# Optimization experiments

Hardware: AMD Instinct MI355X
Metric: run time of the kernel (lower is better)

## Reference

```python
import jax, jax.numpy as jnp
import numpy as np

B, S, C, H, D = 4, 2048, 512, 8, 64
EPS = 1e-5
SCALE = D ** -0.5


def layer_norm(x, w, b):
    m = jnp.mean(x, axis=-1, keepdims=True)
    v = jnp.var(x, axis=-1, keepdims=True)
    return (x - m) * jax.lax.rsqrt(v + EPS) * w + b


def setup_inputs() -> dict:
    key = jax.random.key(0)
    ks = jax.random.split(key, 7)
    s = 0.02
    return {
        "x": jax.random.normal(ks[0], (B, S, C), jnp.float32),
        "Wq": jax.random.normal(ks[1], (C, H * D), jnp.float32) * s,
        "Wk": jax.random.normal(ks[2], (C, H * D), jnp.float32) * s,
        "Wv": jax.random.normal(ks[3], (C, H * D), jnp.float32) * s,
        "Wo": jax.random.normal(ks[4], (H * D, C), jnp.float32) * s,
        "ln1_w": jnp.ones((C,), jnp.float32), "ln1_b": jnp.zeros((C,), jnp.float32),
        "ff_ln1_w": jnp.ones((C,), jnp.float32), "ff_ln1_b": jnp.zeros((C,), jnp.float32),
        "ff_w1": jax.random.normal(ks[5], (C, C), jnp.float32) * s, "ff_b1": jnp.zeros((C,), jnp.float32),
        "ff_ln2_w": jnp.ones((C,), jnp.float32), "ff_ln2_b": jnp.zeros((C,), jnp.float32),
        "ff_w2": jax.random.normal(ks[6], (C, C), jnp.float32) * s, "ff_b2": jnp.zeros((C,), jnp.float32),
        "ln2_w": jnp.ones((C,), jnp.float32), "ln2_b": jnp.zeros((C,), jnp.float32),
    }


def causal_attention(x, Wq, Wk, Wv, Wo):
    # Mathematically identical to the bucketed memory-efficient attention:
    # online-softmax bucketing changes compute order, not the result.
    q = (x @ Wq).reshape(B, S, H, D).transpose(0, 2, 1, 3)  # [B,H,S,D]
    k = (x @ Wk).reshape(B, S, H, D).transpose(0, 2, 1, 3)
    v = (x @ Wv).reshape(B, S, H, D).transpose(0, 2, 1, 3)
    scores = jnp.einsum('bhqd,bhkd->bhqk', q, k) * SCALE  # [B,H,S,S]
    causal = jnp.tril(jnp.ones((S, S), bool))
    scores = jnp.where(causal, scores, jnp.finfo(scores.dtype).min)
    attn = jax.nn.softmax(scores, axis=-1)
    out = jnp.einsum('bhqk,bhkd->bhqd', attn, v)
    out = out.transpose(0, 2, 1, 3).reshape(B, S, H * D)
    return out @ Wo


def reference(x, Wq, Wk, Wv, Wo, ln1_w, ln1_b, ff_ln1_w, ff_ln1_b, ff_w1, ff_b1,
              ff_ln2_w, ff_ln2_b, ff_w2, ff_b2, ln2_w, ln2_b):
    a = causal_attention(x, Wq, Wk, Wv, Wo)
    x_ln = layer_norm(a + x, ln1_w, ln1_b)
    h = layer_norm(x_ln, ff_ln1_w, ff_ln1_b) @ ff_w1 + ff_b1
    h = layer_norm(h, ff_ln2_w, ff_ln2_b) @ ff_w2 + ff_b2
    return layer_norm(h + x_ln, ln2_w, ln2_b)
```

## Files before the change

### kernel.cpp

```cpp
#include <hip/hip_runtime.h>

#define B_ 4
#define S_ 2048
#define C_ 512
#define H_ 8
#define D_ 64
#define M_ 8192

typedef short s8v __attribute__((ext_vector_type(8)));
typedef short s4v __attribute__((ext_vector_type(4)));
typedef float f4v __attribute__((ext_vector_type(4)));
typedef unsigned short u16;
typedef unsigned int u32;

__device__ __forceinline__ u16 f2b(float f) {
    u32 u = __builtin_bit_cast(u32, f);
    u = u + 0x7fffu + ((u >> 16) & 1u);
    return (u16)(u >> 16);
}

__device__ __forceinline__ void gl2lds16(const void* g, void* l) {
    __builtin_amdgcn_global_load_lds(
        (const __attribute__((address_space(1))) void*)g,
        (__attribute__((address_space(3))) void*)l, 16, 0, 0);
}

__global__ __launch_bounds__(256) void conv_k(const float* __restrict__ s,
                                              u16* __restrict__ d) {
    const int i = (blockIdx.x * 256 + threadIdx.x) * 4;
    const float4 v = *(const float4*)&s[i];
    ushort4 o;
    o.x = f2b(v.x); o.y = f2b(v.y); o.z = f2b(v.z); o.w = f2b(v.w);
    *(ushort4*)&d[i] = o;
}

__global__ __launch_bounds__(256) void trconv6_k(const float* __restrict__ s0,
                                                 const float* __restrict__ s1,
                                                 const float* __restrict__ s2,
                                                 const float* __restrict__ s3,
                                                 const float* __restrict__ s4,
                                                 const float* __restrict__ s5,
                                                 u16* __restrict__ d0,
                                                 u16* __restrict__ d1,
                                                 u16* __restrict__ d2,
                                                 u16* __restrict__ d3,
                                                 u16* __restrict__ d4,
                                                 u16* __restrict__ d5)
{
    const float* W; u16* Wt;
    switch (blockIdx.z) {
        case 0: W = s0; Wt = d0; break;
        case 1: W = s1; Wt = d1; break;
        case 2: W = s2; Wt = d2; break;
        case 3: W = s3; Wt = d3; break;
        case 4: W = s4; Wt = d4; break;
        default: W = s5; Wt = d5; break;
    }
    __shared__ float t[32][33];
    const int tx = threadIdx.x & 31, ty = threadIdx.x >> 5;
    const int n0 = blockIdx.x * 32, k0 = blockIdx.y * 32;
    #pragma unroll
    for (int i = 0; i < 4; ++i)
        t[ty + i * 8][tx] = W[(size_t)(k0 + ty + i * 8) * C_ + n0 + tx];
    __syncthreads();
    #pragma unroll
    for (int i = 0; i < 4; ++i)
        Wt[(size_t)(n0 + ty + i * 8) * C_ + k0 + tx] = f2b(t[tx][ty + i * 8]);
}

__global__ __launch_bounds__(256) void vtr_k(const u16* __restrict__ V,
                                             u16* __restrict__ Vt) {
    __shared__ u16 T[64][72];
    const int tid = threadIdx.x;
    const int s0 = blockIdx.x * 64, h = blockIdx.y, b = blockIdx.z;
    const u16* src = V + ((size_t)b * S_) * C_ + h * D_;
    #pragma unroll
    for (int it = 0; it < 2; ++it) {
        const int r = (tid >> 3) + it * 32;
        const int c = (tid & 7) * 8;
        *(s8v*)&T[r][c] = *(const s8v*)&src[(size_t)(s0 + r) * C_ + c];
    }
    __syncthreads();
    u16* dst = Vt + ((size_t)(b * H_ + h)) * D_ * S_;
    #pragma unroll
    for (int it = 0; it < 2; ++it) {
        const int d = (tid >> 3) + it * 32;
        const int sl = (tid & 7) * 8;
        s4v lo, hi;
        #pragma unroll
        for (int i = 0; i < 4; ++i) lo[i] = (short)T[sl + i][d];
        #pragma unroll
        for (int i = 0; i < 4; ++i) hi[i] = (short)T[sl + 4 + i][d];
        const int span = s0 + (sl & ~31);
        const int g0 = (sl & 31) >> 2;
        const int xw = d & 7;
        u16* drow = dst + (size_t)d * S_ + span;
        *(s4v*)&drow[((g0 ^ xw) << 2)]       = lo;
        *(s4v*)&drow[(((g0 + 1) ^ xw) << 2)] = hi;
    }
}

template <bool OB>
__global__ __launch_bounds__(256) void gemm_k(const u16* __restrict__ A,
                                              const u16* __restrict__ Bt,
                                              const float* __restrict__ bias,
                                              void* __restrict__ outv)
{
    __shared__ u16 As[2][8][16][32];
    __shared__ u16 Bs[2][8][16][32];
    const int tid = threadIdx.x;
    const int lane = tid & 63, w = tid >> 6;
    const int q4 = lane >> 4, l16 = lane & 15;
    const int wr = w >> 1, wc = w & 1;
    const int bm = blockIdx.y * 128, bn = blockIdx.x * 128;
    const int lr = lane >> 2, lc = (lane & 3) * 8;

    f4v acc[4][4];
    #pragma unroll
    for (int i = 0; i < 4; ++i)
        #pragma unroll
        for (int j = 0; j < 4; ++j) acc[i][j] = (f4v){0.f, 0.f, 0.f, 0.f};

    #pragma unroll
    for (int r = 0; r < 2; ++r) {
        const int seg = r * 4 + w;
        const int row = seg * 16 + lr;
        gl2lds16(A  + (size_t)(bm + row) * C_ + lc, (char*)As + seg * 1024);
        gl2lds16(Bt + (size_t)(bn + row) * C_ + lc, (char*)Bs + seg * 1024);
    }

    for (int kt = 0; kt < 16; ++kt) {
        __syncthreads();
        const int buf = kt & 1;
        if (kt < 15) {
            const int nb = buf ^ 1, k0 = (kt + 1) * 32;
            #pragma unroll
            for (int r = 0; r < 2; ++r) {
                const int seg = r * 4 + w;
                const int row = seg * 16 + lr;
                gl2lds16(A  + (size_t)(bm + row) * C_ + k0 + lc, (char*)As + nb * 8192 + seg * 1024);
                gl2lds16(Bt + (size_t)(bn + row) * C_ + k0 + lc, (char*)Bs + nb * 8192 + seg * 1024);
            }
        }
        s8v a[4], bf[4];
        #pragma unroll
        for (int i = 0; i < 4; ++i) {
            const int row = wr * 64 + i * 16 + l16;
            a[i] = *(const s8v*)&As[buf][row >> 4][row & 15][q4 * 8];
        }
        #pragma unroll
        for (int j = 0; j < 4; ++j) {
            const int row = wc * 64 + j * 16 + l16;
            bf[j] = *(const s8v*)&Bs[buf][row >> 4][row & 15][q4 * 8];
        }
        #pragma unroll
        for (int i = 0; i < 4; ++i)
            #pragma unroll
            for (int j = 0; j < 4; ++j)
                acc[i][j] = __builtin_amdgcn_mfma_f32_16x16x32_bf16(a[i], bf[j], acc[i][j], 0, 0, 0);
    }

    #pragma unroll
    for (int j = 0; j < 4; ++j) {
        const int n = bn + wc * 64 + j * 16 + l16;
        const float bj = bias ? bias[n] : 0.0f;
        #pragma unroll
        for (int i = 0; i < 4; ++i) {
            const int m = bm + wr * 64 + i * 16 + q4 * 4;
            #pragma unroll
            for (int reg = 0; reg < 4; ++reg) {
                const float vv = acc[i][j][reg] + bj;
                if constexpr (OB) ((u16*)outv)[(size_t)(m + reg) * C_ + n] = f2b(vv);
                else              ((float*)outv)[(size_t)(m + reg) * C_ + n] = vv;
            }
        }
    }
}

__global__ __launch_bounds__(256) void qkv_k(const u16* __restrict__ A,
                                             const u16* __restrict__ Wq,
                                             const u16* __restrict__ Wk,
                                             const u16* __restrict__ Wv,
                                             u16* __restrict__ oq,
                                             u16* __restrict__ ok,
                                             u16* __restrict__ ov)
{
    __shared__ u16 As[2][8][16][32];
    __shared__ u16 Bs[2][8][16][32];
    const int tid = threadIdx.x;
    const int lane = tid & 63, w = tid >> 6;
    const int q4 = lane >> 4, l16 = lane & 15;
    const int wr = w >> 1, wc = w & 1;
    const int nt = blockIdx.x, which = nt >> 2;
    const u16* Bt = which == 0 ? Wq : (which == 1 ? Wk : Wv);
    u16* outp = which == 0 ? oq : (which == 1 ? ok : ov);
    const int bm = blockIdx.y * 128, bn = (nt & 3) * 128;
    const int lr = lane >> 2, lc = (lane & 3) * 8;

    f4v acc[4][4];
    #pragma unroll
    for (int i = 0; i < 4; ++i)
        #pragma unroll
        for (int j = 0; j < 4; ++j) acc[i][j] = (f4v){0.f, 0.f, 0.f, 0.f};

    #pragma unroll
    for (int r = 0; r < 2; ++r) {
        const int seg = r * 4 + w;
        const int row = seg * 16 + lr;
        gl2lds16(A  + (size_t)(bm + row) * C_ + lc, (char*)As + seg * 1024);
        gl2lds16(Bt + (size_t)(bn + row) * C_ + lc, (char*)Bs + seg * 1024);
    }
    for (int kt = 0; kt < 16; ++kt) {
        __syncthreads();
        const int buf = kt & 1;
        if (kt < 15) {
            const int nb = buf ^ 1, k0 = (kt + 1) * 32;
            #pragma unroll
            for (int r = 0; r < 2; ++r) {
                const int seg = r * 4 + w;
                const int row = seg * 16 + lr;
                gl2lds16(A  + (size_t)(bm + row) * C_ + k0 + lc, (char*)As + nb * 8192 + seg * 1024);
                gl2lds16(Bt + (size_t)(bn + row) * C_ + k0 + lc, (char*)Bs + nb * 8192 + seg * 1024);
            }
        }
        s8v a[4], bf[4];
        #pragma unroll
        for (int i = 0; i < 4; ++i) {
            const int row = wr * 64 + i * 16 + l16;
            a[i] = *(const s8v*)&As[buf][row >> 4][row & 15][q4 * 8];
        }
        #pragma unroll
        for (int j = 0; j < 4; ++j) {
            const int row = wc * 64 + j * 16 + l16;
            bf[j] = *(const s8v*)&Bs[buf][row >> 4][row & 15][q4 * 8];
        }
        #pragma unroll
        for (int i = 0; i < 4; ++i)
            #pragma unroll
            for (int j = 0; j < 4; ++j)
                acc[i][j] = __builtin_amdgcn_mfma_f32_16x16x32_bf16(a[i], bf[j], acc[i][j], 0, 0, 0);
    }
    #pragma unroll
    for (int j = 0; j < 4; ++j) {
        const int n = bn + wc * 64 + j * 16 + l16;
        #pragma unroll
        for (int i = 0; i < 4; ++i) {
            const int m = bm + wr * 64 + i * 16 + q4 * 4;
            #pragma unroll
            for (int reg = 0; reg < 4; ++reg)
                outp[(size_t)(m + reg) * C_ + n] = f2b(acc[i][j][reg]);
        }
    }
}

template <bool OB>
__global__ __launch_bounds__(256) void ln_k(const float* __restrict__ in,
                                            const float* __restrict__ res,
                                            const float* __restrict__ w,
                                            const float* __restrict__ bb,
                                            void* __restrict__ outv)
{
    const int lane = threadIdx.x & 63;
    const int row  = blockIdx.x * 4 + (threadIdx.x >> 6);
    const float* p = in + (size_t)row * C_;
    float4 v0 = *(const float4*)&p[lane * 4];
    float4 v1 = *(const float4*)&p[256 + lane * 4];
    if (res) {
        const float* rp = res + (size_t)row * C_;
        const float4 r0 = *(const float4*)&rp[lane * 4];
        const float4 r1 = *(const float4*)&rp[256 + lane * 4];
        v0.x += r0.x; v0.y += r0.y; v0.z += r0.z; v0.w += r0.w;
        v1.x += r1.x; v1.y += r1.y; v1.z += r1.z; v1.w += r1.w;
    }
    float s  = v0.x + v0.y + v0.z + v0.w + v1.x + v1.y + v1.z + v1.w;
    float ss = v0.x*v0.x + v0.y*v0.y + v0.z*v0.z + v0.w*v0.w
             + v1.x*v1.x + v1.y*v1.y + v1.z*v1.z + v1.w*v1.w;
    #pragma unroll
    for (int off = 32; off >= 1; off >>= 1) {
        s  += __shfl_xor(s, off);
        ss += __shfl_xor(ss, off);
    }
    const float mean = s * (1.0f / C_);
    const float var  = ss * (1.0f / C_) - mean * mean;
    const float rstd = rsqrtf(var + 1e-5f);

    const float4 w0 = *(const float4*)&w[lane * 4];
    const float4 w1 = *(const float4*)&w[256 + lane * 4];
    const float4 b0 = *(const float4*)&bb[lane * 4];
    const float4 b1 = *(const float4*)&bb[256 + lane * 4];
    float4 o0, o1;
    o0.x = (v0.x - mean) * rstd * w0.x + b0.x;
    o0.y = (v0.y - mean) * rstd * w0.y + b0.y;
    o0.z = (v0.z - mean) * rstd * w0.z + b0.z;
    o0.w = (v0.w - mean) * rstd * w0.w + b0.w;
    o1.x = (v1.x - mean) * rstd * w1.x + b1.x;
    o1.y = (v1.y - mean) * rstd * w1.y + b1.y;
    o1.z = (v1.z - mean) * rstd * w1.z + b1.z;
    o1.w = (v1.w - mean) * rstd * w1.w + b1.w;
    if constexpr (OB) {
        u16* op = (u16*)outv + (size_t)row * C_;
        ushort4 u0, u1;
        u0.x = f2b(o0.x); u0.y = f2b(o0.y); u0.z = f2b(o0.z); u0.w = f2b(o0.w);
        u1.x = f2b(o1.x); u1.y = f2b(o1.y); u1.z = f2b(o1.z); u1.w = f2b(o1.w);
        *(ushort4*)&op[lane * 4]       = u0;
        *(ushort4*)&op[256 + lane * 4] = u1;
    } else {
        float* op = (float*)outv + (size_t)row * C_;
        *(float4*)&op[lane * 4]       = o0;
        *(float4*)&op[256 + lane * 4] = o1;
    }
}

__global__ __launch_bounds__(256) void attn_k(const u16* __restrict__ Q,
                                              const u16* __restrict__ K,
                                              const u16* __restrict__ Vt,
                                              u16* __restrict__ O)
{
    __shared__ u16 Ks[2][2][64][32];
    __shared__ u16 Vs[2][2][64][32];
    const int tid = threadIdx.x;
    const int lane = tid & 63, w = tid >> 6;
    const int q4 = lane >> 4, l16 = lane & 15;
    const int x = blockIdx.x, h = blockIdx.y, b = blockIdx.z;
    const int qb = (x & 1) ? 31 - (x >> 1) : (x >> 1);
    const size_t base  = ((size_t)b * S_) * C_ + h * D_;
    const size_t basev = ((size_t)(b * H_ + h)) * D_ * S_;
    const int lr = lane >> 2, lc = (lane & 3) * 8;

    s8v qf[2];
    #pragma unroll
    for (int kh = 0; kh < 2; ++kh)
        qf[kh] = *(const s8v*)&Q[base + (size_t)(qb * 64 + w * 16 + l16) * C_ + kh * 32 + q4 * 8];

    #pragma unroll
    for (int r = 0; r < 2; ++r) {
        const int seg = r * 4 + w;
        const int row = (seg & 3) * 16 + lr;
        const int kh = seg >> 2;
        gl2lds16(K  + base  + (size_t)row * C_ + kh * 32 + lc, (char*)Ks + seg * 1024);
        gl2lds16(Vt + basev + (size_t)row * S_ + kh * 32 + lc, (char*)Vs + seg * 1024);
    }

    f4v o[4];
    float lp[4] = {0.f, 0.f, 0.f, 0.f};
    #pragma unroll
    for (int j = 0; j < 4; ++j) o[j] = (f4v){0.f, 0.f, 0.f, 0.f};

    const int qrow = w * 16 + l16;
    for (int kb = 0; kb <= qb; ++kb) {
        __syncthreads();
        const int buf = kb & 1;
        if (kb < qb) {
            const int nb = buf ^ 1, kn = kb + 1;
            #pragma unroll
            for (int r = 0; r < 2; ++r) {
                const int seg = r * 4 + w;
                const int row = (seg & 3) * 16 + lr;
                const int kh = seg >> 2;
                gl2lds16(K  + base  + (size_t)(kn * 64 + row) * C_ + kh * 32 + lc,
                         (char*)Ks + nb * 8192 + seg * 1024);
                gl2lds16(Vt + basev + (size_t)row * S_ + kn * 64 + kh * 32 + lc,
                         (char*)Vs + nb * 8192 + seg * 1024);
            }
        }

        f4v sc[4];
        #pragma unroll
        for (int j = 0; j < 4; ++j) sc[j] = (f4v){0.f, 0.f, 0.f, 0.f};
        #pragma unroll
        for (int kh = 0; kh < 2; ++kh) {
            #pragma unroll
            for (int j = 0; j < 4; ++j) {
                const s8v kf = *(const s8v*)&Ks[buf][kh][j * 16 + l16][q4 * 8];
                sc[j] = __builtin_amdgcn_mfma_f32_16x16x32_bf16(kf, qf[kh], sc[j], 0, 0, 0);
            }
        }

        const bool diag = (kb == qb);
        s4v pa[4];
        #pragma unroll
        for (int j = 0; j < 4; ++j) {
            float ps = 0.0f;
            #pragma unroll
            for (int reg = 0; reg < 4; ++reg) {
                float t = fmaf(sc[j][reg], 0.18033688011112043f, -11.541560327111707f);
                if (diag && (j * 16 + q4 * 4 + reg) > qrow) t = -128.0f;
                const float p = exp2f(t);
                ps += p;
                pa[j][reg] = (short)(__builtin_bit_cast(u32, p) >> 16);
            }
            lp[j] += ps;
        }

        #pragma unroll
        for (int c = 0; c < 4; ++c) {
            const int gh = (((c & 1) * 4 + q4) ^ (l16 & 7)) * 4;
            #pragma unroll
            for (int dj = 0; dj < 4; ++dj) {
                const s4v vb = *(const s4v*)&Vs[buf][c >> 1][dj * 16 + l16][gh];
                o[dj] = __builtin_amdgcn_mfma_f32_16x16x16bf16_1k(pa[c], vb, o[dj], 0, 0, 0);
            }
        }
    }

    float lt = (lp[0] + lp[1]) + (lp[2] + lp[3]);
    lt += __shfl_xor(lt, 16);
    lt += __shfl_xor(lt, 32);
    #pragma unroll
    for (int reg = 0; reg < 4; ++reg) {
        const float inv = 1.0f / __shfl(lt, q4 * 4 + reg);
        const size_t rowoff = base + (size_t)(qb * 64 + w * 16 + q4 * 4 + reg) * C_;
        #pragma unroll
        for (int dj = 0; dj < 4; ++dj)
            O[rowoff + dj * 16 + l16] = f2b(o[dj][reg] * inv);
    }
}

extern "C" void kernel_launch(void* const* d_in, const int* in_sizes, int n_in,
                              void* d_out, int out_size, void* d_ws, size_t ws_size,
                              hipStream_t stream)
{
    const float* x       = (const float*)d_in[0];
    const float* Wq      = (const float*)d_in[1];
    const float* Wk      = (const float*)d_in[2];
    const float* Wv      = (const float*)d_in[3];
    const float* Wo      = (const float*)d_in[4];
    const float* ln1_w   = (const float*)d_in[5];
    const float* ln1_b   = (const float*)d_in[6];
    const float* ffln1_w = (const float*)d_in[7];
    const float* ffln1_b = (const float*)d_in[8];
    const float* ff_w1   = (const float*)d_in[9];
    const float* ff_b1   = (const float*)d_in[10];
    const float* ffln2_w = (const float*)d_in[11];
    const float* ffln2_b = (const float*)d_in[12];
    const float* ff_w2   = (const float*)d_in[13];
    const float* ff_b2   = (const float*)d_in[14];
    const float* ln2_w   = (const float*)d_in[15];
    const float* ln2_b   = (const float*)d_in[16];
    float* out = (float*)d_out;

    const size_t MC = (size_t)M_ * C_;
    const size_t WW = (size_t)C_ * C_;
    u16* xb   = (u16*)d_ws;
    u16* WqT  = xb + MC;
    u16* WkT  = WqT + WW;
    u16* WvT  = WkT + WW;
    u16* WoT  = WvT + WW;
    u16* W1T  = WoT + WW;
    u16* W2T  = W1T + WW;
    u16* qbuf = W2T + WW;
    u16* kbuf = qbuf + MC;
    u16* vbuf = kbuf + MC;
    u16* vtbuf= vbuf + MC;
    u16* abuf = xb;
    float* tf  = (float*)qbuf;
    float* xln = (float*)vbuf;
    u16*   lnb = xb;

    const dim3 gg(C_ / 128, M_ / 128);
    const dim3 gq(12, M_ / 128);
    const dim3 ga(32, H_, B_);
    const dim3 gv(S_ / 64, H_, B_);
    const dim3 gt(16, 16, 6);
    const int  gl = M_ / 4;

    conv_k<<<MC / 1024, 256, 0, stream>>>(x, xb);
    trconv6_k<<<gt, 256, 0, stream>>>(Wq, Wk, Wv, Wo, ff_w1, ff_w2,
                                      WqT, WkT, WvT, WoT, W1T, W2T);

    qkv_k<<<gq, 256, 0, stream>>>(xb, WqT, WkT, WvT, qbuf, kbuf, vbuf);
    vtr_k<<<gv, 256, 0, stream>>>(vbuf, vtbuf);
    attn_k<<<ga, 256, 0, stream>>>(qbuf, kbuf, vtbuf, abuf);
    gemm_k<false><<<gg, 256, 0, stream>>>(abuf, WoT, nullptr, tf);
    ln_k<false><<<gl, 256, 0, stream>>>(tf, x, ln1_w, ln1_b, xln);
    ln_k<true><<<gl, 256, 0, stream>>>(xln, nullptr, ffln1_w, ffln1_b, lnb);
    gemm_k<false><<<gg, 256, 0, stream>>>(lnb, W1T, ff_b1, tf);
    ln_k<true><<<gl, 256, 0, stream>>>(tf, nullptr, ffln2_w, ffln2_b, lnb);
    gemm_k<false><<<gg, 256, 0, stream>>>(lnb, W2T, ff_b2, tf);
    ln_k<false><<<gl, 256, 0, stream>>>(tf, xln, ln2_w, ln2_b, out);
}
```

Measured before the change: 270.5 us.

## Fuse V transpose into QKV, merge LayerNorms, retile GEMM and attention

The QKV kernel now writes V directly in the swizzled transposed layout, which removes the separate vtr_k kernel. Two consecutive LayerNorms are fused into one kernel that writes both the fp32 residual and the bf16 normalized output. The output GEMMs use 64x128 tiles, doubling the grid for better CU occupancy. Attention now handles 128 query rows per block as two 16-row groups per wave so each K/V tile is reused twice, and only the diagonal tiles apply the causal mask. The trade-offs are more registers per attention wave, fewer attention blocks, and scattered 8-byte writes for V.

```diff
diff --git a/kernel.cpp b/kernel.cpp
--- a/kernel.cpp
+++ b/kernel.cpp
@@ -68,65 +68,31 @@
         Wt[(size_t)(n0 + ty + i * 8) * C_ + k0 + tx] = f2b(t[tx][ty + i * 8]);
 }
 
-__global__ __launch_bounds__(256) void vtr_k(const u16* __restrict__ V,
-                                             u16* __restrict__ Vt) {
-    __shared__ u16 T[64][72];
-    const int tid = threadIdx.x;
-    const int s0 = blockIdx.x * 64, h = blockIdx.y, b = blockIdx.z;
-    const u16* src = V + ((size_t)b * S_) * C_ + h * D_;
-    #pragma unroll
-    for (int it = 0; it < 2; ++it) {
-        const int r = (tid >> 3) + it * 32;
-        const int c = (tid & 7) * 8;
-        *(s8v*)&T[r][c] = *(const s8v*)&src[(size_t)(s0 + r) * C_ + c];
-    }
-    __syncthreads();
-    u16* dst = Vt + ((size_t)(b * H_ + h)) * D_ * S_;
-    #pragma unroll
-    for (int it = 0; it < 2; ++it) {
-        const int d = (tid >> 3) + it * 32;
-        const int sl = (tid & 7) * 8;
-        s4v lo, hi;
-        #pragma unroll
-        for (int i = 0; i < 4; ++i) lo[i] = (short)T[sl + i][d];
-        #pragma unroll
-        for (int i = 0; i < 4; ++i) hi[i] = (short)T[sl + 4 + i][d];
-        const int span = s0 + (sl & ~31);
-        const int g0 = (sl & 31) >> 2;
-        const int xw = d & 7;
-        u16* drow = dst + (size_t)d * S_ + span;
-        *(s4v*)&drow[((g0 ^ xw) << 2)]       = lo;
-        *(s4v*)&drow[(((g0 + 1) ^ xw) << 2)] = hi;
-    }
-}
-
 template <bool OB>
 __global__ __launch_bounds__(256) void gemm_k(const u16* __restrict__ A,
                                               const u16* __restrict__ Bt,
                                               const float* __restrict__ bias,
                                               void* __restrict__ outv)
 {
-    __shared__ u16 As[2][8][16][32];
+    __shared__ u16 As[2][4][16][32];
     __shared__ u16 Bs[2][8][16][32];
     const int tid = threadIdx.x;
     const int lane = tid & 63, w = tid >> 6;
     const int q4 = lane >> 4, l16 = lane & 15;
-    const int wr = w >> 1, wc = w & 1;
-    const int bm = blockIdx.y * 128, bn = blockIdx.x * 128;
+    const int bm = blockIdx.y * 64, bn = blockIdx.x * 128;
     const int lr = lane >> 2, lc = (lane & 3) * 8;
 
-    f4v acc[4][4];
+    f4v acc[4][2];
     #pragma unroll
     for (int i = 0; i < 4; ++i)
         #pragma unroll
-        for (int j = 0; j < 4; ++j) acc[i][j] = (f4v){0.f, 0.f, 0.f, 0.f};
-
+        for (int j = 0; j < 2; ++j) acc[i][j] = (f4v){0.f, 0.f, 0.f, 0.f};
+
+    gl2lds16(A + (size_t)(bm + w * 16 + lr) * C_ + lc, (char*)As + w * 1024);
     #pragma unroll
     for (int r = 0; r < 2; ++r) {
-        const int seg = r * 4 + w;
-        const int row = seg * 16 + lr;
-        gl2lds16(A  + (size_t)(bm + row) * C_ + lc, (char*)As + seg * 1024);
-        gl2lds16(Bt + (size_t)(bn + row) * C_ + lc, (char*)Bs + seg * 1024);
+        const int seg = w * 2 + r;
+        gl2lds16(Bt + (size_t)(bn + seg * 16 + lr) * C_ + lc, (char*)Bs + seg * 1024);
     }
 
     for (int kt = 0; kt < 16; ++kt) {
@@ -134,39 +100,37 @@
         const int buf = kt & 1;
         if (kt < 15) {
             const int nb = buf ^ 1, k0 = (kt + 1) * 32;
+            gl2lds16(A + (size_t)(bm + w * 16 + lr) * C_ + k0 + lc,
+                     (char*)As + nb * 4096 + w * 1024);
             #pragma unroll
             for (int r = 0; r < 2; ++r) {
-                const int seg = r * 4 + w;
-                const int row = seg * 16 + lr;
-                gl2lds16(A  + (size_t)(bm + row) * C_ + k0 + lc, (char*)As + nb * 8192 + seg * 1024);
-                gl2lds16(Bt + (size_t)(bn + row) * C_ + k0 + lc, (char*)Bs + nb * 8192 + seg * 1024);
-            }
-        }
-        s8v a[4], bf[4];
+                const int seg = w * 2 + r;
+                gl2lds16(Bt + (size_t)(bn + seg * 16 + lr) * C_ + k0 + lc,
+                         (char*)Bs + nb * 8192 + seg * 1024);
+            }
+        }
+        s8v a[4], bfr[2];
+        #pragma unroll
+        for (int i = 0; i < 4; ++i) a[i] = *(const s8v*)&As[buf][i][l16][q4 * 8];
+        #pragma unroll
+        for (int j = 0; j < 2; ++j) {
+            const int row = w * 32 + j * 16 + l16;
+            bfr[j] = *(const s8v*)&Bs[buf][row >> 4][row & 15][q4 * 8];
+        }
+        #pragma unroll
+        for (int i = 0; i < 4; ++i)
+            #pragma unroll
+            for (int j = 0; j < 2; ++j)
+                acc[i][j] = __builtin_amdgcn_mfma_f32_16x16x32_bf16(a[i], bfr[j], acc[i][j], 0, 0, 0);
+    }
+
+    #pragma unroll
+    for (int j = 0; j < 2; ++j) {
+        const int n = bn + w * 32 + j * 16 + l16;
+        const float bj = bias ? bias[n] : 0.0f;
         #pragma unroll
         for (int i = 0; i < 4; ++i) {
-            const int row = wr * 64 + i * 16 + l16;
-            a[i] = *(const s8v*)&As[buf][row >> 4][row & 15][q4 * 8];
-        }
-        #pragma unroll
-        for (int j = 0; j < 4; ++j) {
-            const int row = wc * 64 + j * 16 + l16;
-            bf[j] = *(const s8v*)&Bs[buf][row >> 4][row & 15][q4 * 8];
-        }
-        #pragma unroll
-        for (int i = 0; i < 4; ++i)
-            #pragma unroll
-            for (int j = 0; j < 4; ++j)
-                acc[i][j] = __builtin_amdgcn_mfma_f32_16x16x32_bf16(a[i], bf[j], acc[i][j], 0, 0, 0);
-    }
-
-    #pragma unroll
-    for (int j = 0; j < 4; ++j) {
-        const int n = bn + wc * 64 + j * 16 + l16;
-        const float bj = bias ? bias[n] : 0.0f;
-        #pragma unroll
-        for (int i = 0; i < 4; ++i) {
-            const int m = bm + wr * 64 + i * 16 + q4 * 4;
+            const int m = bm + i * 16 + q4 * 4;
             #pragma unroll
             for (int reg = 0; reg < 4; ++reg) {
                 const float vv = acc[i][j][reg] + bj;
@@ -183,7 +147,7 @@
                                              const u16* __restrict__ Wv,
                                              u16* __restrict__ oq,
                                              u16* __restrict__ ok,
-                                             u16* __restrict__ ov)
+                                             u16* __restrict__ ovt)
 {
     __shared__ u16 As[2][8][16][32];
     __shared__ u16 Bs[2][8][16][32];
@@ -193,7 +157,6 @@
     const int wr = w >> 1, wc = w & 1;
     const int nt = blockIdx.x, which = nt >> 2;
     const u16* Bt = which == 0 ? Wq : (which == 1 ? Wk : Wv);
-    u16* outp = which == 0 ? oq : (which == 1 ? ok : ov);
     const int bm = blockIdx.y * 128, bn = (nt & 3) * 128;
     const int lr = lane >> 2, lc = (lane & 3) * 8;
 
@@ -240,15 +203,38 @@
             for (int j = 0; j < 4; ++j)
                 acc[i][j] = __builtin_amdgcn_mfma_f32_16x16x32_bf16(a[i], bf[j], acc[i][j], 0, 0, 0);
     }
-    #pragma unroll
-    for (int j = 0; j < 4; ++j) {
-        const int n = bn + wc * 64 + j * 16 + l16;
-        #pragma unroll
-        for (int i = 0; i < 4; ++i) {
-            const int m = bm + wr * 64 + i * 16 + q4 * 4;
-            #pragma unroll
-            for (int reg = 0; reg < 4; ++reg)
-                outp[(size_t)(m + reg) * C_ + n] = f2b(acc[i][j][reg]);
+
+    if (which != 2) {
+        u16* outp = which == 0 ? oq : ok;
+        #pragma unroll
+        for (int j = 0; j < 4; ++j) {
+            const int n = bn + wc * 64 + j * 16 + l16;
+            #pragma unroll
+            for (int i = 0; i < 4; ++i) {
+                const int m = bm + wr * 64 + i * 16 + q4 * 4;
+                #pragma unroll
+                for (int reg = 0; reg < 4; ++reg)
+                    outp[(size_t)(m + reg) * C_ + n] = f2b(acc[i][j][reg]);
+            }
+        }
+    } else {
+        const int bglob = bm >> 11;
+        const int sbase = bm & (S_ - 1);
+        #pragma unroll
+        for (int j = 0; j < 4; ++j) {
+            const int n = bn + wc * 64 + j * 16 + l16;
+            const int h = n >> 6, d = n & 63;
+            u16* vrow = ovt + ((size_t)(bglob * H_ + h) * D_ + d) * S_;
+            const int xw = d & 7;
+            #pragma unroll
+            for (int i = 0; i < 4; ++i) {
+                const int s = sbase + wr * 64 + i * 16 + q4 * 4;
+                const int pg = ((s & 31) >> 2) ^ xw;
+                s4v pv;
+                #pragma unroll
+                for (int reg = 0; reg < 4; ++reg) pv[reg] = (short)f2b(acc[i][j][reg]);
+                *(s4v*)&vrow[(s & ~31) + (pg << 2)] = pv;
+            }
         }
     }
 }
@@ -311,6 +297,86 @@
     }
 }
 
+__global__ __launch_bounds__(256) void ln2x_k(const float* __restrict__ in,
+                                              const float* __restrict__ res,
+                                              const float* __restrict__ w1,
+                                              const float* __restrict__ b1,
+                                              const float* __restrict__ w2,
+                                              const float* __restrict__ b2,
+                                              float* __restrict__ out1,
+                                              u16* __restrict__ out2)
+{
+    const int lane = threadIdx.x & 63;
+    const int row  = blockIdx.x * 4 + (threadIdx.x >> 6);
+    const float* p  = in  + (size_t)row * C_;
+    const float* rp = res + (size_t)row * C_;
+    float4 v0 = *(const float4*)&p[lane * 4];
+    float4 v1 = *(const float4*)&p[256 + lane * 4];
+    {
+        const float4 r0 = *(const float4*)&rp[lane * 4];
+        const float4 r1 = *(const float4*)&rp[256 + lane * 4];
+        v0.x += r0.x; v0.y += r0.y; v0.z += r0.z; v0.w += r0.w;
+        v1.x += r1.x; v1.y += r1.y; v1.z += r1.z; v1.w += r1.w;
+    }
+    float s  = v0.x + v0.y + v0.z + v0.w + v1.x + v1.y + v1.z + v1.w;
+    float ss = v0.x*v0.x + v0.y*v0.y + v0.z*v0.z + v0.w*v0.w
+             + v1.x*v1.x + v1.y*v1.y + v1.z*v1.z + v1.w*v1.w;
+    #pragma unroll
+    for (int off = 32; off >= 1; off >>= 1) {
+        s  += __shfl_xor(s, off);
+        ss += __shfl_xor(ss, off);
+    }
+    float mean = s * (1.0f / C_);
+    float var  = ss * (1.0f / C_) - mean * mean;
+    float rstd = rsqrtf(var + 1e-5f);
+
+    const float4 wA0 = *(const float4*)&w1[lane * 4];
+    const float4 wA1 = *(const float4*)&w1[256 + lane * 4];
+    const float4 bA0 = *(const float4*)&b1[lane * 4];
+    const float4 bA1 = *(const float4*)&b1[256 + lane * 4];
+    float4 y0, y1v;
+    y0.x  = (v0.x - mean) * rstd * wA0.x + bA0.x;
+    y0.y  = (v0.y - mean) * rstd * wA0.y + bA0.y;
+    y0.z  = (v0.z - mean) * rstd * wA0.z + bA0.z;
+    y0.w  = (v0.w - mean) * rstd * wA0.w + bA0.w;
+    y1v.x = (v1.x - mean) * rstd * wA1.x + bA1.x;
+    y1v.y = (v1.y - mean) * rstd * wA1.y + bA1.y;
+    y1v.z = (v1.z - mean) * rstd * wA1.z + bA1.z;
+    y1v.w = (v1.w - mean) * rstd * wA1.w + bA1.w;
+    float* op1 = out1 + (size_t)row * C_;
+    *(float4*)&op1[lane * 4]       = y0;
+    *(float4*)&op1[256 + lane * 4] = y1v;
+
+    s  = y0.x + y0.y + y0.z + y0.w + y1v.x + y1v.y + y1v.z + y1v.w;
+    ss = y0.x*y0.x + y0.y*y0.y + y0.z*y0.z + y0.w*y0.w
+       + y1v.x*y1v.x + y1v.y*y1v.y + y1v.z*y1v.z + y1v.w*y1v.w;
+    #pragma unroll
+    for (int off = 32; off >= 1; off >>= 1) {
+        s  += __shfl_xor(s, off);
+        ss += __shfl_xor(ss, off);
+    }
+    mean = s * (1.0f / C_);
+    var  = ss * (1.0f / C_) - mean * mean;
+    rstd = rsqrtf(var + 1e-5f);
+
+    const float4 wB0 = *(const float4*)&w2[lane * 4];
+    const float4 wB1 = *(const float4*)&w2[256 + lane * 4];
+    const float4 bB0 = *(const float4*)&b2[lane * 4];
+    const float4 bB1 = *(const float4*)&b2[256 + lane * 4];
+    ushort4 u0, u1;
+    u0.x = f2b((y0.x - mean) * rstd * wB0.x + bB0.x);
+    u0.y = f2b((y0.y - mean) * rstd * wB0.y + bB0.y);
+    u0.z = f2b((y0.z - mean) * rstd * wB0.z + bB0.z);
+    u0.w = f2b((y0.w - mean) * rstd * wB0.w + bB0.w);
+    u1.x = f2b((y1v.x - mean) * rstd * wB1.x + bB1.x);
+    u1.y = f2b((y1v.y - mean) * rstd * wB1.y + bB1.y);
+    u1.z = f2b((y1v.z - mean) * rstd * wB1.z + bB1.z);
+    u1.w = f2b((y1v.w - mean) * rstd * wB1.w + bB1.w);
+    u16* op2 = out2 + (size_t)row * C_;
+    *(ushort4*)&op2[lane * 4]       = u0;
+    *(ushort4*)&op2[256 + lane * 4] = u1;
+}
+
 __global__ __launch_bounds__(256) void attn_k(const u16* __restrict__ Q,
                                               const u16* __restrict__ K,
                                               const u16* __restrict__ Vt,
@@ -322,15 +388,18 @@
     const int lane = tid & 63, w = tid >> 6;
     const int q4 = lane >> 4, l16 = lane & 15;
     const int x = blockIdx.x, h = blockIdx.y, b = blockIdx.z;
-    const int qb = (x & 1) ? 31 - (x >> 1) : (x >> 1);
+    const int qb = (x & 1) ? 15 - (x >> 1) : (x >> 1);
     const size_t base  = ((size_t)b * S_) * C_ + h * D_;
     const size_t basev = ((size_t)(b * H_ + h)) * D_ * S_;
     const int lr = lane >> 2, lc = (lane & 3) * 8;
 
-    s8v qf[2];
-    #pragma unroll
-    for (int kh = 0; kh < 2; ++kh)
-        qf[kh] = *(const s8v*)&Q[base + (size_t)(qb * 64 + w * 16 + l16) * C_ + kh * 32 + q4 * 8];
+    s8v qf[2][2];
+    #pragma unroll
+    for (int g = 0; g < 2; ++g)
+        #pragma unroll
+        for (int kh = 0; kh < 2; ++kh)
+            qf[g][kh] = *(const s8v*)&Q[base + (size_t)(qb * 128 + w * 32 + g * 16 + l16) * C_
+                                        + kh * 32 + q4 * 8];
 
     #pragma unroll
     for (int r = 0; r < 2; ++r) {
@@ -341,16 +410,18 @@
         gl2lds16(Vt + basev + (size_t)row * S_ + kh * 32 + lc, (char*)Vs + seg * 1024);
     }
 
-    f4v o[4];
-    float lp[4] = {0.f, 0.f, 0.f, 0.f};
-    #pragma unroll
-    for (int j = 0; j < 4; ++j) o[j] = (f4v){0.f, 0.f, 0.f, 0.f};
-
-    const int qrow = w * 16 + l16;
-    for (int kb = 0; kb <= qb; ++kb) {
+    f4v o[2][4];
+    float lp[2][4];
+    #pragma unroll
+    for (int g = 0; g < 2; ++g)
+        #pragma unroll
+        for (int j = 0; j < 4; ++j) { o[g][j] = (f4v){0.f, 0.f, 0.f, 0.f}; lp[g][j] = 0.f; }
+
+    const int nt = 2 * qb + 2;
+    for (int kb = 0; kb < nt; ++kb) {
         __syncthreads();
         const int buf = kb & 1;
-        if (kb < qb) {
+        if (kb + 1 < nt) {
             const int nb = buf ^ 1, kn = kb + 1;
             #pragma unroll
             for (int r = 0; r < 2; ++r) {
@@ -364,32 +435,57 @@
             }
         }
 
-        f4v sc[4];
-        #pragma unroll
-        for (int j = 0; j < 4; ++j) sc[j] = (f4v){0.f, 0.f, 0.f, 0.f};
+        f4v sc[2][4];
+        #pragma unroll
+        for (int g = 0; g < 2; ++g)
+            #pragma unroll
+            for (int j = 0; j < 4; ++j) sc[g][j] = (f4v){0.f, 0.f, 0.f, 0.f};
         #pragma unroll
         for (int kh = 0; kh < 2; ++kh) {
             #pragma unroll
             for (int j = 0; j < 4; ++j) {
                 const s8v kf = *(const s8v*)&Ks[buf][kh][j * 16 + l16][q4 * 8];
-                sc[j] = __builtin_amdgcn_mfma_f32_16x16x32_bf16(kf, qf[kh], sc[j], 0, 0, 0);
-            }
-        }
-
-        const bool diag = (kb == qb);
-        s4v pa[4];
-        #pragma unroll
-        for (int j = 0; j < 4; ++j) {
-            float ps = 0.0f;
-            #pragma unroll
-            for (int reg = 0; reg < 4; ++reg) {
-                float t = fmaf(sc[j][reg], 0.18033688011112043f, -11.541560327111707f);
-                if (diag && (j * 16 + q4 * 4 + reg) > qrow) t = -128.0f;
-                const float p = exp2f(t);
-                ps += p;
-                pa[j][reg] = (short)(__builtin_bit_cast(u32, p) >> 16);
-            }
-            lp[j] += ps;
+                #pragma unroll
+                for (int g = 0; g < 2; ++g)
+                    sc[g][j] = __builtin_amdgcn_mfma_f32_16x16x32_bf16(kf, qf[g][kh], sc[g][j], 0, 0, 0);
+            }
+        }
+
+        s4v pa[2][4];
+        if (kb >= 2 * qb) {
+            #pragma unroll
+            for (int g = 0; g < 2; ++g) {
+                const int qrow = qb * 128 + w * 32 + g * 16 + l16;
+                #pragma unroll
+                for (int j = 0; j < 4; ++j) {
+                    float ps = 0.0f;
+                    #pragma unroll
+                    for (int reg = 0; reg < 4; ++reg) {
+                        const int key = kb * 64 + j * 16 + q4 * 4 + reg;
+                        float t = fmaf(sc[g][j][reg], 0.18033688011112043f, -11.541560327111707f);
+                        if (key > qrow) t = -128.0f;
+                        const float p = exp2f(t);
+                        ps += p;
+                        pa[g][j][reg] = (short)(__builtin_bit_cast(u32, p) >> 16);
+                    }
+                    lp[g][j] += ps;
+                }
+            }
+        } else {
+            #pragma unroll
+            for (int g = 0; g < 2; ++g)
+                #pragma unroll
+                for (int j = 0; j < 4; ++j) {
+                    float ps = 0.0f;
+                    #pragma unroll
+                    for (int reg = 0; reg < 4; ++reg) {
+                        const float p = exp2f(fmaf(sc[g][j][reg], 0.18033688011112043f,
+                                                   -11.541560327111707f));
+                        ps += p;
+                        pa[g][j][reg] = (short)(__builtin_bit_cast(u32, p) >> 16);
+                    }
+                    lp[g][j] += ps;
+                }
         }
 
         #pragma unroll
@@ -398,21 +494,26 @@
             #pragma unroll
             for (int dj = 0; dj < 4; ++dj) {
                 const s4v vb = *(const s4v*)&Vs[buf][c >> 1][dj * 16 + l16][gh];
-                o[dj] = __builtin_amdgcn_mfma_f32_16x16x16bf16_1k(pa[c], vb, o[dj], 0, 0, 0);
-            }
-        }
-    }
-
-    float lt = (lp[0] + lp[1]) + (lp[2] + lp[3]);
-    lt += __shfl_xor(lt, 16);
-    lt += __shfl_xor(lt, 32);
-    #pragma unroll
-    for (int reg = 0; reg < 4; ++reg) {
-        const float inv = 1.0f / __shfl(lt, q4 * 4 + reg);
-        const size_t rowoff = base + (size_t)(qb * 64 + w * 16 + q4 * 4 + reg) * C_;
-        #pragma unroll
-        for (int dj = 0; dj < 4; ++dj)
-            O[rowoff + dj * 16 + l16] = f2b(o[dj][reg] * inv);
+                #pragma unroll
+                for (int g = 0; g < 2; ++g)
+                    o[g][dj] = __builtin_amdgcn_mfma_f32_16x16x16bf16_1k(pa[g][c], vb, o[g][dj], 0, 0, 0);
+            }
+        }
+    }
+
+    #pragma unroll
+    for (int g = 0; g < 2; ++g) {
+        float lt = (lp[g][0] + lp[g][1]) + (lp[g][2] + lp[g][3]);
+        lt += __shfl_xor(lt, 16);
+        lt += __shfl_xor(lt, 32);
+        #pragma unroll
+        for (int reg = 0; reg < 4; ++reg) {
+            const float inv = 1.0f / __shfl(lt, q4 * 4 + reg);
+            const size_t rowoff = base + (size_t)(qb * 128 + w * 32 + g * 16 + q4 * 4 + reg) * C_;
+            #pragma unroll
+            for (int dj = 0; dj < 4; ++dj)
+                O[rowoff + dj * 16 + l16] = f2b(o[g][dj][reg] * inv);
+        }
     }
 }
 
@@ -457,10 +558,9 @@
     float* xln = (float*)vbuf;
     u16*   lnb = xb;
 
-    const dim3 gg(C_ / 128, M_ / 128);
+    const dim3 gg(C_ / 128, M_ / 64);
     const dim3 gq(12, M_ / 128);
-    const dim3 ga(32, H_, B_);
-    const dim3 gv(S_ / 64, H_, B_);
+    const dim3 ga(16, H_, B_);
     const dim3 gt(16, 16, 6);
     const int  gl = M_ / 4;
 
@@ -468,12 +568,11 @@
     trconv6_k<<<gt, 256, 0, stream>>>(Wq, Wk, Wv, Wo, ff_w1, ff_w2,
                                       WqT, WkT, WvT, WoT, W1T, W2T);
 
-    qkv_k<<<gq, 256, 0, stream>>>(xb, WqT, WkT, WvT, qbuf, kbuf, vbuf);
-    vtr_k<<<gv, 256, 0, stream>>>(vbuf, vtbuf);
+    qkv_k<<<gq, 256, 0, stream>>>(xb, WqT, WkT, WvT, qbuf, kbuf, vtbuf);
     attn_k<<<ga, 256, 0, stream>>>(qbuf, kbuf, vtbuf, abuf);
     gemm_k<false><<<gg, 256, 0, stream>>>(abuf, WoT, nullptr, tf);
-    ln_k<false><<<gl, 256, 0, stream>>>(tf, x, ln1_w, ln1_b, xln);
-    ln_k<true><<<gl, 256, 0, stream>>>(xln, nullptr, ffln1_w, ffln1_b, lnb);
+    ln2x_k<<<gl, 256, 0, stream>>>(tf, x, ln1_w, ln1_b, ffln1_w, ffln1_b,
+                                   xln, lnb);
     gemm_k<false><<<gg, 256, 0, stream>>>(lnb, W1T, ff_b1, tf);
     ln_k<true><<<gl, 256, 0, stream>>>(tf, nullptr, ffln2_w, ffln2_b, lnb);
     gemm_k<false><<<gg, 256, 0, stream>>>(lnb, W2T, ff_b2, tf);
```

After: 274.9 us. Within noise of the previous version (+1.6%).
